# Performance work log

Hardware: AMD Instinct MI355X
Metric: run time of the kernel (lower is better)

## Reference

```python
import math
import jax, jax.numpy as jnp
import numpy as np

B, T, M, S, D, H = 16, 512, 8, 32, 256, 4
HD = D // H


def setup_inputs() -> dict:
    key = jax.random.key(0)
    ks = jax.random.split(key, 16)
    w = 1.0 / math.sqrt(D)
    return {
        'q_temporal': jax.random.normal(ks[0], (B, T, M, D), jnp.float32),
        'q_static': jax.random.normal(ks[1], (B, S, D), jnp.float32),
        'k_temporal': jax.random.normal(ks[2], (B, T, M, D), jnp.float32),
        'v_temporal': jax.random.normal(ks[3], (B, T, M, D), jnp.float32),
        'k_static': jax.random.normal(ks[4], (B, S, D), jnp.float32),
        'v_static': jax.random.normal(ks[5], (B, S, D), jnp.float32),
        'q_w': jax.random.normal(ks[6], (D, D), jnp.float32) * w,
        'q_b': jax.random.normal(ks[7], (D,), jnp.float32) * w,
        'k_w': jax.random.normal(ks[8], (D, D), jnp.float32) * w,
        'k_b': jax.random.normal(ks[9], (D,), jnp.float32) * w,
        'v_w': jax.random.normal(ks[10], (D, D), jnp.float32) * w,
        'v_b': jax.random.normal(ks[11], (D,), jnp.float32) * w,
        'o_w': jax.random.normal(ks[12], (D, D), jnp.float32) * w,
        'o_b': jax.random.normal(ks[13], (D,), jnp.float32) * w,
        'mask_temporal': jax.random.randint(ks[14], (B, T, M), 0, 2).astype(jnp.int32),
        'mask_fcst': jax.random.randint(ks[15], (B, T, M), 0, 2).astype(jnp.int32),
        'mask_static': jnp.ones((B, S), jnp.int32),
    }


def _lin(x, w, b):
    # torch.nn.Linear: y = x @ W^T + b
    return x @ w.T + b


def reference(q_temporal, q_static, k_temporal, v_temporal, k_static, v_static,
              q_w, q_b, k_w, k_b, v_w, v_b, o_w, o_b,
              mask_temporal, mask_fcst, mask_static):
    scale = 1.0 / math.sqrt(HD)

    def heads5(x):  # [B,T,M,D] -> [B,H,T,M,HD]
        return x.reshape(B, T, M, H, HD).transpose(0, 3, 1, 2, 4)

    def heads3(x):  # [B,S,D] -> [B,H,S,HD]
        return x.reshape(B, -1, H, HD).transpose(0, 2, 1, 3)

    Qt = heads5(_lin(q_temporal, q_w, q_b))
    Kt = heads5(_lin(k_temporal, k_w, k_b))
    Vt = heads5(_lin(v_temporal, v_w, v_b))
    Qs = heads3(_lin(q_static, q_w, q_b))
    Ks = heads3(_lin(k_static, k_w, k_b))
    Vs = heads3(_lin(v_static, v_w, v_b))

    # additive masks: 0 where valid (==1), -inf where padded
    mt = jnp.where(mask_temporal == 1, 0.0, -jnp.inf).astype(Qt.dtype)  # [B,T,M]
    ms = jnp.where(mask_static == 1, 0.0, -jnp.inf).astype(Qt.dtype)    # [B,S]

    # ---- temporal query branch ----
    # temp_temp: per-timestep modality-vs-modality attention, column key mask
    Qt_Kt = jnp.einsum('bhtmd,bhtnd->bhtmn', Qt, Kt) * scale + mt[:, None, :, None, :]
    # temp_static: temporal queries vs static keys
    Qt_Ks = jnp.einsum('bhtmd,bhsd->bhtms', Qt, Ks) * scale + ms[:, None, None, None, :]
    tw = jax.nn.softmax(jnp.concatenate([Qt_Kt, Qt_Ks], axis=-1), axis=-1)  # [B,H,T,M,M+S]
    QKV_t = (jnp.einsum('bhtmn,bhtnd->bhtmd', tw[..., :M], Vt)
             + jnp.einsum('bhtms,bhsd->bhtmd', tw[..., M:], Vs))
    out_t = _lin(QKV_t.transpose(0, 2, 3, 1, 4).reshape(B, T, M, D), o_w, o_b)

    # ---- static query branch ----
    Ktf = Kt.reshape(B, H, T * M, HD)  # flatten (T,M) key axis
    Vtf = Vt.reshape(B, H, T * M, HD)
    Qs_Kt = jnp.einsum('bhqd,bhkd->bhqk', Qs, Ktf) * scale + mt.reshape(B, 1, 1, T * M)
    Qs_Ks = jnp.einsum('bhqd,bhsd->bhqs', Qs, Ks) * scale + ms[:, None, None, :]
    sw = jax.nn.softmax(jnp.concatenate([Qs_Kt, Qs_Ks], axis=-1), axis=-1)  # [B,H,S,T*M+S]
    QKV_s = (jnp.einsum('bhqk,bhkd->bhqd', sw[..., :T * M], Vtf)
             + jnp.einsum('bhqs,bhsd->bhqd', sw[..., T * M:], Vs))
    out_s = _lin(QKV_s.transpose(0, 2, 1, 3).reshape(B, S, D), o_w, o_b)

    return (out_t, out_s, tw, sw)
```

## Files before the change

### kernel.cpp

```cpp
#include <hip/hip_runtime.h>

#define B_   16
#define T_   512
#define M_   8
#define S_   32
#define D_   256
#define H_   4
#define HD_  64
#define TM_  4096
#define NKT  40
#define NKS  4128

typedef unsigned short u16;
typedef __attribute__((ext_vector_type(8))) short bf16x8;
typedef __attribute__((ext_vector_type(4))) float f32x4;

__device__ __forceinline__ u16 f2b(float f) {
    union { float f; unsigned u; } v; v.f = f;
    unsigned r = v.u + 0x7FFF + ((v.u >> 16) & 1);
    return (u16)(r >> 16);
}
__device__ __forceinline__ float blo(unsigned u) {
    union { unsigned i; float f; } v; v.i = u << 16; return v.f;
}
__device__ __forceinline__ float bhi(unsigned u) {
    union { unsigned i; float f; } v; v.i = u & 0xFFFF0000u; return v.f;
}
__device__ __forceinline__ float b2f(u16 u) {
    union { unsigned i; float f; } v; v.i = ((unsigned)u) << 16; return v.f;
}
__device__ __forceinline__ unsigned pack2(float lo, float hi) {
    return (unsigned)f2b(lo) | ((unsigned)f2b(hi) << 16);
}
__device__ __forceinline__ uint4 cvt8(float4 a, float4 b) {
    uint4 r;
    r.x = pack2(a.x, a.y); r.y = pack2(a.z, a.w);
    r.z = pack2(b.x, b.y); r.w = pack2(b.z, b.w);
    return r;
}

template<int XBF, int OUTF32>
__device__ __forceinline__ void gemm_body(const void* __restrict__ Xv,
                                          const float* __restrict__ W,
                                          const float* __restrict__ bias,
                                          void* __restrict__ Yv,
                                          int bx, u16* sA, u16* sB)
{
    const int tid = threadIdx.x;
    const size_t r0 = (size_t)bx * 64;
    const int wave = tid >> 6, lane = tid & 63;
    const int rbase = lane & 15, kseg = (lane >> 4) * 8;
    const int arow = tid >> 2, aseg = tid & 3;

    f32x4 acc[4][4];
#pragma unroll
    for (int i = 0; i < 4; ++i)
#pragma unroll
        for (int j = 0; j < 4; ++j) acc[i][j] = (f32x4){0, 0, 0, 0};

#define LOAD_A(k0, dst)                                                          \
    if (XBF) dst = *(const uint4*)((const u16*)Xv + (r0 + arow) * 256 + (k0) + aseg * 8); \
    else {                                                                       \
        const float* gA = (const float*)Xv + (r0 + arow) * 256 + (k0) + aseg * 8; \
        dst = cvt8(*(const float4*)gA, *(const float4*)(gA + 4));                \
    }
#define LOAD_B(k0, dst)                                                          \
    _Pragma("unroll")                                                            \
    for (int i = 0; i < 4; ++i) {                                                \
        const int s = i * 256 + tid;                                             \
        const float* gB = W + (size_t)(s >> 2) * 256 + (k0) + (s & 3) * 8;       \
        dst[i] = cvt8(*(const float4*)gB, *(const float4*)(gB + 4));             \
    }

    {
        uint4 aC, bC[4];
        LOAD_A(0, aC)
        LOAD_B(0, bC)
        *(uint4*)(sA + tid * 8) = aC;
#pragma unroll
        for (int i = 0; i < 4; ++i)
            *(uint4*)(sB + (i * 256 + tid) * 8) = bC[i];
    }

    for (int k = 0; k < 8; ++k) {
        const int cur = k & 1;
        uint4 aN, bN[4];
        if (k < 7) {
            LOAD_A((k + 1) * 32, aN)
            LOAD_B((k + 1) * 32, bN)
        }
        __syncthreads();
        const u16* A = sA + cur * 2048;
        const u16* Bb = sB + cur * 8192;
        bf16x8 a[4], b[4];
#pragma unroll
        for (int f = 0; f < 4; ++f)
            a[f] = *(const bf16x8*)(A + (f * 16 + rbase) * 32 + kseg);
#pragma unroll
        for (int f = 0; f < 4; ++f)
            b[f] = *(const bf16x8*)(Bb + (wave * 64 + f * 16 + rbase) * 32 + kseg);
#pragma unroll
        for (int rf = 0; rf < 4; ++rf)
#pragma unroll
            for (int cf = 0; cf < 4; ++cf)
                acc[rf][cf] = __builtin_amdgcn_mfma_f32_16x16x32_bf16(
                    a[rf], b[cf], acc[rf][cf], 0, 0, 0);
        if (k < 7) {
            u16* A1 = sA + (cur ^ 1) * 2048;
            u16* B1 = sB + (cur ^ 1) * 8192;
            *(uint4*)(A1 + tid * 8) = aN;
#pragma unroll
            for (int i = 0; i < 4; ++i)
                *(uint4*)(B1 + (i * 256 + tid) * 8) = bN[i];
        }
    }
#undef LOAD_A
#undef LOAD_B

    const int orow = (lane >> 4) * 4, ocol = lane & 15;
#pragma unroll
    for (int cf = 0; cf < 4; ++cf) {
        const int col = wave * 64 + cf * 16 + ocol;
        const float bv = bias[col];
#pragma unroll
        for (int rf = 0; rf < 4; ++rf)
#pragma unroll
            for (int r = 0; r < 4; ++r) {
                const size_t row = r0 + rf * 16 + orow + r;
                const float y = acc[rf][cf][r] + bv;
                if (OUTF32) ((float*)Yv)[row * 256 + col] = y;
                else        ((u16*) Yv)[row * 256 + col] = f2b(y);
            }
    }
}

template<int XBF, int OUTF32>
__global__ __launch_bounds__(256) void k_gemm_m(const void* __restrict__ Xv,
                                                const float* __restrict__ W,
                                                const float* __restrict__ bias,
                                                void* __restrict__ Yv)
{
    __shared__ __align__(16) u16 sA[2 * 2048];
    __shared__ __align__(16) u16 sB[2 * 8192];
    gemm_body<XBF, OUTF32>(Xv, W, bias, Yv, blockIdx.x, sA, sB);
}

__global__ __launch_bounds__(256) void k_gemm_qkv(
    const float* __restrict__ X0, const float* __restrict__ X1, const float* __restrict__ X2,
    const float* __restrict__ W0, const float* __restrict__ W1, const float* __restrict__ W2,
    const float* __restrict__ b0, const float* __restrict__ b1, const float* __restrict__ b2,
    u16* __restrict__ Y0, u16* __restrict__ Y1, u16* __restrict__ Y2)
{
    __shared__ __align__(16) u16 sA[2 * 2048];
    __shared__ __align__(16) u16 sB[2 * 8192];
    const int sel = blockIdx.y;
    const float* X = sel == 0 ? X0 : sel == 1 ? X1 : X2;
    const float* W = sel == 0 ? W0 : sel == 1 ? W1 : W2;
    const float* bb = sel == 0 ? b0 : sel == 1 ? b1 : b2;
    u16* Y = sel == 0 ? Y0 : sel == 1 ? Y1 : Y2;
    gemm_body<0, 0>(X, W, bb, Y, blockIdx.x, sA, sB);
}

__global__ __launch_bounds__(256) void k_attn_t(
    const u16* __restrict__ Qt, const u16* __restrict__ Kt, const u16* __restrict__ Vt,
    const u16* __restrict__ Ks, const u16* __restrict__ Vs,
    const int* __restrict__ maskT, const int* __restrict__ maskS,
    float* __restrict__ tw, u16* __restrict__ qkvt)
{
    const int tp = blockIdx.x, b = blockIdx.y;
    const int t0 = tp * 2;
    __shared__ __align__(16) u16 sQ [4 * 2 * 16 * 32];
    __shared__ __align__(16) u16 sKT[4 * 2 * 16 * 32];
    __shared__ __align__(16) u16 sKS[4 * 2 * 32 * 32];
    __shared__ __align__(16) u16 sVT[4 * 64 * 72];
    __shared__ __align__(16) u16 sP [4 * 16 * 72];
    __shared__ int smT[2][8];
    __shared__ int smS[32];
    const int tid = threadIdx.x;

#pragma unroll
    for (int i = 0; i < 2; ++i) {
        const int fl = tid + i * 256;
        const int r = fl >> 5, c32 = fl & 31;
        const int h = c32 >> 3, ks = (c32 >> 2) & 1, seg = c32 & 3;
        const size_t src = (((size_t)b * T_ + t0 + (r >> 3)) * 8 + (r & 7)) * 256 + c32 * 8;
        const int dst = h * 1024 + ks * 512 + r * 32 + seg * 8;
        *(uint4*)(sQ  + dst) = *(const uint4*)(Qt + src);
        *(uint4*)(sKT + dst) = *(const uint4*)(Kt + src);
    }
#pragma unroll
    for (int i = 0; i < 4; ++i) {
        const int fl = tid + i * 256;
        const int r = fl >> 5, c32 = fl & 31;
        const int h = c32 >> 3, ks = (c32 >> 2) & 1, seg = c32 & 3;
        *(uint4*)(sKS + h * 2048 + ks * 1024 + r * 32 + seg * 8) =
            *(const uint4*)(Ks + ((size_t)b * S_ + r) * 256 + c32 * 8);
    }
    {
        const int key = tid & 63, dg = tid >> 6;
        const u16* vrow = nullptr;
        if (key < 16)      vrow = Vt + (((size_t)b * T_ + t0 + (key >> 3)) * 8 + (key & 7)) * 256;
        else if (key < 48) vrow = Vs + ((size_t)b * S_ + (key - 16)) * 256;
#pragma unroll
        for (int i = 0; i < 8; ++i) {
            const int dseg = dg * 8 + i;
            uint4 v = {0, 0, 0, 0};
            if (vrow) v = *(const uint4*)(vrow + dseg * 8);
            const int h = dseg >> 3, dl0 = (dseg & 7) * 8;
            const u16* pv = (const u16*)&v;
#pragma unroll
            for (int j = 0; j < 8; ++j)
                sVT[h * 4608 + (dl0 + j) * 72 + key] = pv[j];
        }
    }
    if (tid < 16) smT[tid >> 3][tid & 7] =
        maskT[((size_t)b * T_ + t0 + (tid >> 3)) * 8 + (tid & 7)];
    if (tid < 32) smS[tid] = maskS[b * S_ + tid];
    __syncthreads();

    const int h = tid >> 6, lane = tid & 63;
    const int c = lane & 15, g = lane >> 4, th = g >> 1;

    f32x4 at = {0,0,0,0}, as0 = {0,0,0,0}, as1 = {0,0,0,0};
#pragma unroll
    for (int ks = 0; ks < 2; ++ks) {
        bf16x8 aq = *(const bf16x8*)(sQ  + h * 1024 + ks * 512 + c * 32 + g * 8);
        bf16x8 bt = *(const bf16x8*)(sKT + h * 1024 + ks * 512 + c * 32 + g * 8);
        bf16x8 b0 = *(const bf16x8*)(sKS + h * 2048 + ks * 1024 + c * 32 + g * 8);
        bf16x8 b1 = *(const bf16x8*)(sKS + h * 2048 + ks * 1024 + 512 + c * 32 + g * 8);
        at  = __builtin_amdgcn_mfma_f32_16x16x32_bf16(aq, bt, at, 0, 0, 0);
        as0 = __builtin_amdgcn_mfma_f32_16x16x32_bf16(aq, b0, as0, 0, 0, 0);
        as1 = __builtin_amdgcn_mfma_f32_16x16x32_bf16(aq, b1, as1, 0, 0, 0);
    }

    const int vt = ((c >> 3) == th) ? smT[th][c & 7] : 0;
    const int v0 = smS[c], v1 = smS[16 + c];
    float st[4], s0[4], s1[4], mx[4];
#pragma unroll
    for (int r = 0; r < 4; ++r) {
        st[r] = vt ? at[r]  * 0.125f : -1e30f;
        s0[r] = v0 ? as0[r] * 0.125f : -1e30f;
        s1[r] = v1 ? as1[r] * 0.125f : -1e30f;
        mx[r] = fmaxf(fmaxf(st[r], s0[r]), s1[r]);
    }
#pragma unroll
    for (int o = 1; o < 16; o <<= 1)
#pragma unroll
        for (int r = 0; r < 4; ++r) mx[r] = fmaxf(mx[r], __shfl_xor(mx[r], o));
    float pt[4], p0[4], p1[4], sum[4];
#pragma unroll
    for (int r = 0; r < 4; ++r) {
        pt[r] = __expf(st[r] - mx[r]);
        p0[r] = __expf(s0[r] - mx[r]);
        p1[r] = __expf(s1[r] - mx[r]);
        sum[r] = pt[r] + p0[r] + p1[r];
    }
#pragma unroll
    for (int o = 1; o < 16; o <<= 1)
#pragma unroll
        for (int r = 0; r < 4; ++r) sum[r] += __shfl_xor(sum[r], o);
#pragma unroll
    for (int r = 0; r < 4; ++r) {
        const float inv = 1.0f / sum[r];
        pt[r] *= inv; p0[r] *= inv; p1[r] *= inv;
    }

#pragma unroll
    for (int r = 0; r < 4; ++r) {
        const int row = g * 4 + r;
        const int tt = t0 + (row >> 3), m = row & 7;
        float* twp = tw + ((((size_t)b * H_ + h) * T_ + tt) * 8 + m) * NKT;
        if ((c >> 3) == th) twp[c & 7] = pt[r];
        twp[8 + c]  = p0[r];
        twp[24 + c] = p1[r];
        u16* sp = sP + h * 1152 + row * 72;
        sp[c]      = f2b(pt[r]);
        sp[16 + c] = f2b(p0[r]);
        sp[32 + c] = f2b(p1[r]);
        sp[48 + c] = 0;
    }

    f32x4 o4[4] = {{0,0,0,0}, {0,0,0,0}, {0,0,0,0}, {0,0,0,0}};
#pragma unroll
    for (int ks = 0; ks < 2; ++ks) {
        bf16x8 pa = *(const bf16x8*)(sP + h * 1152 + c * 72 + ks * 32 + g * 8);
#pragma unroll
        for (int dt = 0; dt < 4; ++dt) {
            bf16x8 pb = *(const bf16x8*)(sVT + h * 4608 + (dt * 16 + c) * 72 + ks * 32 + g * 8);
            o4[dt] = __builtin_amdgcn_mfma_f32_16x16x32_bf16(pa, pb, o4[dt], 0, 0, 0);
        }
    }
#pragma unroll
    for (int dt = 0; dt < 4; ++dt)
#pragma unroll
        for (int r = 0; r < 4; ++r) {
            const int row = g * 4 + r;
            const int tt = t0 + (row >> 3), m = row & 7;
            qkvt[(((size_t)b * T_ + tt) * 8 + m) * 256 + h * 64 + dt * 16 + c] = f2b(o4[dt][r]);
        }
}

__global__ __launch_bounds__(256) void k_attn_s_scores(
    const u16* __restrict__ Qs, const u16* __restrict__ Kt, const u16* __restrict__ Ks,
    const int* __restrict__ maskT, const int* __restrict__ maskS,
    float* __restrict__ raw)
{
    const int ch = blockIdx.x, h = blockIdx.y, b = blockIdx.z;
    const int nk = (ch < 32) ? 128 : 32;
    const int k0 = ch * 128;
    __shared__ __align__(16) u16 sQ[2 * 32 * 32];
    __shared__ __align__(16) u16 sK[2 * 128 * 32];
    __shared__ int sM[128];
    const int tid = threadIdx.x;

    {   const int q = tid >> 3, c8 = tid & 7;
        const int ks = c8 >> 2, seg = c8 & 3;
        *(uint4*)(sQ + ks * 1024 + q * 32 + seg * 8) =
            *(const uint4*)(Qs + ((size_t)b * S_ + q) * 256 + h * 64 + c8 * 8);
    }
#pragma unroll
    for (int i = 0; i < 4; ++i) {
        const int fl = tid + i * 256;
        const int key = fl >> 3, c8 = fl & 7;
        const int ks = c8 >> 2, seg = c8 & 3;
        if (key < nk) {
            const u16* src = (ch < 32)
                ? (Kt + ((size_t)b * TM_ + k0 + key) * 256 + h * 64 + c8 * 8)
                : (Ks + ((size_t)b * S_  +      key) * 256 + h * 64 + c8 * 8);
            *(uint4*)(sK + ks * 4096 + key * 32 + seg * 8) = *(const uint4*)src;
        }
    }
    if (tid < nk) sM[tid] = (ch < 32) ? maskT[(size_t)b * TM_ + k0 + tid]
                                      : maskS[b * S_ + tid];
    __syncthreads();

    const int w = tid >> 6, lane = tid & 63;
    if (w * 32 >= nk) return;
    const int c = lane & 15, g = lane >> 4;

    f32x4 acc[2][2] = {{{0,0,0,0}, {0,0,0,0}}, {{0,0,0,0}, {0,0,0,0}}};
#pragma unroll
    for (int ks = 0; ks < 2; ++ks) {
        bf16x8 a0 = *(const bf16x8*)(sQ + ks * 1024 +        c * 32 + g * 8);
        bf16x8 a1 = *(const bf16x8*)(sQ + ks * 1024 + 512 +  c * 32 + g * 8);
        bf16x8 b0 = *(const bf16x8*)(sK + ks * 4096 + (w * 32 +      c) * 32 + g * 8);
        bf16x8 b1 = *(const bf16x8*)(sK + ks * 4096 + (w * 32 + 16 + c) * 32 + g * 8);
        acc[0][0] = __builtin_amdgcn_mfma_f32_16x16x32_bf16(a0, b0, acc[0][0], 0, 0, 0);
        acc[0][1] = __builtin_amdgcn_mfma_f32_16x16x32_bf16(a0, b1, acc[0][1], 0, 0, 0);
        acc[1][0] = __builtin_amdgcn_mfma_f32_16x16x32_bf16(a1, b0, acc[1][0], 0, 0, 0);
        acc[1][1] = __builtin_amdgcn_mfma_f32_16x16x32_bf16(a1, b1, acc[1][1], 0, 0, 0);
    }
#pragma unroll
    for (int rt = 0; rt < 2; ++rt)
#pragma unroll
        for (int ct = 0; ct < 2; ++ct) {
            const int kl = w * 32 + ct * 16 + c;
            const float madd = sM[kl] ? 0.f : -1e30f;
#pragma unroll
            for (int r = 0; r < 4; ++r) {
                const int q = rt * 16 + g * 4 + r;
                raw[(((size_t)b * H_ + h) * S_ + q) * NKS + k0 + kl] =
                    acc[rt][ct][r] * 0.125f + madd;
            }
        }
}

__global__ __launch_bounds__(256) void k_attn_s_softmax(
    const float* __restrict__ raw, float* __restrict__ sw)
{
    const int q = blockIdx.x, h = blockIdx.y, b = blockIdx.z;
    __shared__ float sRow[NKS];
    __shared__ float red[8];
    const int tid = threadIdx.x;
    const size_t base = (((size_t)b * H_ + h) * S_ + q) * NKS;

    float mx = -1e30f;
    for (int i = tid; i < NKS; i += 256) {
        const float v = raw[base + i];
        sRow[i] = v;
        mx = fmaxf(mx, v);
    }
    for (int o = 32; o; o >>= 1) mx = fmaxf(mx, __shfl_xor(mx, o));
    if ((tid & 63) == 0) red[tid >> 6] = mx;
    __syncthreads();
    mx = fmaxf(fmaxf(red[0], red[1]), fmaxf(red[2], red[3]));

    float sum = 0.f;
    for (int i = tid; i < NKS; i += 256) {
        const float e = __expf(sRow[i] - mx);
        sRow[i] = e;
        sum += e;
    }
    for (int o = 32; o; o >>= 1) sum += __shfl_xor(sum, o);
    if ((tid & 63) == 0) red[4 + (tid >> 6)] = sum;
    __syncthreads();
    sum = (red[4] + red[5]) + (red[6] + red[7]);
    const float inv = 1.0f / sum;

    for (int i = tid; i < NKS; i += 256)
        sw[base + i] = sRow[i] * inv;
}

__global__ __launch_bounds__(256) void k_attn_s_pv_part(
    const float* __restrict__ w, const u16* __restrict__ Vt, const u16* __restrict__ Vs,
    float* __restrict__ part)
{
    const int ch = blockIdx.x, h = blockIdx.y, b = blockIdx.z;
    const int nk = (ch < 32) ? 128 : 32;
    const int k0 = ch * 128;
    __shared__ float sW[32][132];
    __shared__ __align__(16) u16 sV[128 * 64];
    const int tid = threadIdx.x;

#pragma unroll
    for (int i = 0; i < 4; ++i) {
        const int fl = tid + i * 256;
        const int q = fl >> 5, k4 = fl & 31;
        if (k4 * 4 < nk)
            *(float4*)&sW[q][k4 * 4] =
                *(const float4*)(w + (((size_t)b * H_ + h) * S_ + q) * NKS + k0 + k4 * 4);
    }
#pragma unroll
    for (int i = 0; i < 4; ++i) {
        const int fl = tid + i * 256;
        const int key = fl >> 3, pp = fl & 7;
        if (key < nk) {
            const u16* src = (ch < 32)
                ? (Vt + ((size_t)b * TM_ + k0 + key) * D_ + h * HD_ + pp * 8)
                : (Vs + ((size_t)b * S_  +      key) * D_ + h * HD_ + pp * 8);
            ((uint4*)sV)[fl] = *(const uint4*)src;
        }
    }
    __syncthreads();

    const int d = tid & 63, qg = tid >> 6;
    float acc[8] = {0,0,0,0,0,0,0,0};
    for (int kk = 0; kk < nk; kk += 4) {
        const float v0 = b2f(sV[(kk + 0) * 64 + d]);
        const float v1 = b2f(sV[(kk + 1) * 64 + d]);
        const float v2 = b2f(sV[(kk + 2) * 64 + d]);
        const float v3 = b2f(sV[(kk + 3) * 64 + d]);
#pragma unroll
        for (int j = 0; j < 8; ++j) {
            const float4 wv = *(const float4*)&sW[qg * 8 + j][kk];
            acc[j] += wv.x * v0 + wv.y * v1 + wv.z * v2 + wv.w * v3;
        }
    }

    float* pb = part + (((size_t)ch * B_ + b) * H_ + h) * 2048;
#pragma unroll
    for (int j = 0; j < 8; ++j)
        pb[(qg * 8 + j) * 64 + d] = acc[j];
}

__global__ __launch_bounds__(256) void k_attn_s_pv_red(
    const float* __restrict__ part, u16* __restrict__ qkvs)
{
    const int h = blockIdx.x, b = blockIdx.y;
    const int tid = threadIdx.x;
    for (int i = tid; i < 2048; i += 256) {
        float s = 0.f;
#pragma unroll
        for (int c = 0; c < 33; ++c)
            s += part[(((size_t)c * B_ + b) * H_ + h) * 2048 + i];
        const int q = i >> 6, d = i & 63;
        qkvs[((size_t)b * S_ + q) * D_ + h * HD_ + d] = f2b(s);
    }
}

extern "C" void kernel_launch(void* const* d_in, const int* in_sizes, int n_in,
                              void* d_out, int out_size, void* d_ws, size_t ws_size,
                              hipStream_t stream)
{
    const float* q_t = (const float*)d_in[0];
    const float* q_s = (const float*)d_in[1];
    const float* k_t = (const float*)d_in[2];
    const float* v_t = (const float*)d_in[3];
    const float* k_s = (const float*)d_in[4];
    const float* v_s = (const float*)d_in[5];
    const float* q_w = (const float*)d_in[6];
    const float* q_b = (const float*)d_in[7];
    const float* k_w = (const float*)d_in[8];
    const float* k_b = (const float*)d_in[9];
    const float* v_w = (const float*)d_in[10];
    const float* v_b = (const float*)d_in[11];
    const float* o_w = (const float*)d_in[12];
    const float* o_b = (const float*)d_in[13];
    const int* maskT = (const int*)d_in[14];
    const int* maskS = (const int*)d_in[16];
    float* out = (float*)d_out;

    char* ws = (char*)d_ws;
    u16*   Kt   = (u16*)(ws + 0);
    u16*   Vt   = (u16*)(ws + 33554432);
    u16*   QKVt = (u16*)(ws + 67108864);
    float* part = (float*)(ws + 67108864);
    u16*   Qs   = (u16*)(ws + 100663296);
    u16*   Ks   = (u16*)(ws + 100925440);
    u16*   Vs   = (u16*)(ws + 101187584);
    u16*   QKVs = (u16*)(ws + 101449728);
    u16*   Qt   = (u16*)(ws + 101711872);
    float* raw  = (float*)(ws + 101711872);
    if (ws_size < 135528448) return;

    float* out_t = out;
    float* out_s = out + 16777216;
    float* tw    = out + 16908288;
    float* sw    = out + 27394048;

    const dim3 blk(256);
    k_gemm_qkv<<<dim3(1024, 3), blk, 0, stream>>>(q_t, k_t, v_t, q_w, k_w, v_w,
                                                  q_b, k_b, v_b, Qt, Kt, Vt);
    k_gemm_qkv<<<dim3(8, 3),    blk, 0, stream>>>(q_s, k_s, v_s, q_w, k_w, v_w,
                                                  q_b, k_b, v_b, Qs, Ks, Vs);

    k_attn_t<<<dim3(256, 16), blk, 0, stream>>>(Qt, Kt, Vt, Ks, Vs, maskT, maskS, tw, QKVt);

    k_gemm_m<1,1><<<dim3(1024), blk, 0, stream>>>(QKVt, o_w, o_b, out_t);

    k_attn_s_scores<<<dim3(33, 4, 16), blk, 0, stream>>>(Qs, Kt, Ks, maskT, maskS, raw);
    k_attn_s_softmax<<<dim3(32, 4, 16), blk, 0, stream>>>(raw, sw);
    k_attn_s_pv_part<<<dim3(33, 4, 16), blk, 0, stream>>>(sw, Vt, Vs, part);
    k_attn_s_pv_red<<<dim3(4, 16), blk, 0, stream>>>(part, QKVs);

    k_gemm_m<1,1><<<dim3(8),    blk, 0, stream>>>(QKVs, o_w, o_b, out_s);
}
```

Measured before the change: 284.3 us.

## Pre-convert weights to bf16 and stage GEMM tiles with direct global-to-LDS loads

Adds a small kernel converting projection weights to bf16 once, so GEMM blocks load bf16 weights via global_load_lds directly into shared memory instead of loading and converting fp32 per block. The bf16 A operand is also staged asynchronously, and the bf16 output epilogue is routed through LDS for coalesced 16-byte stores. This adds extra conversion launches and workspace aliasing that depends on kernel ordering.

New measurement: 257.5 us. -9.4%, faster.

```diff
diff --git a/kernel.cpp b/kernel.cpp
--- a/kernel.cpp
+++ b/kernel.cpp
@@ -39,13 +39,33 @@
     return r;
 }
 
+#define GLL16(g, l) __builtin_amdgcn_global_load_lds( \
+    (const __attribute__((address_space(1))) void*)(g), \
+    (__attribute__((address_space(3))) void*)(l), 16, 0, 0)
+
+__global__ __launch_bounds__(256) void k_cvt_w(const float* __restrict__ W0,
+                                               const float* __restrict__ W1,
+                                               const float* __restrict__ W2,
+                                               u16* __restrict__ dst)
+{
+    const int sel = blockIdx.y;
+    const float* W = sel == 0 ? W0 : sel == 1 ? W1 : W2;
+    u16* d = dst + sel * 65536;
+    const int i0 = (blockIdx.x * 256 + threadIdx.x) * 8;
+    const float4 a = *(const float4*)(W + i0);
+    const float4 b = *(const float4*)(W + i0 + 4);
+    *(uint4*)(d + i0) = cvt8(a, b);
+}
+
 template<int XBF, int OUTF32>
 __device__ __forceinline__ void gemm_body(const void* __restrict__ Xv,
-                                          const float* __restrict__ W,
+                                          const u16* __restrict__ Wb,
                                           const float* __restrict__ bias,
                                           void* __restrict__ Yv,
-                                          int bx, u16* sA, u16* sB)
-{
+                                          int bx, u16* smem)
+{
+    u16* sA = smem;
+    u16* sB = smem + 4096;
     const int tid = threadIdx.x;
     const size_t r0 = (size_t)bx * 64;
     const int wave = tid >> 6, lane = tid & 63;
@@ -58,39 +78,38 @@
 #pragma unroll
         for (int j = 0; j < 4; ++j) acc[i][j] = (f32x4){0, 0, 0, 0};
 
-#define LOAD_A(k0, dst)                                                          \
-    if (XBF) dst = *(const uint4*)((const u16*)Xv + (r0 + arow) * 256 + (k0) + aseg * 8); \
-    else {                                                                       \
+#define LOAD_A_F32(k0, dst) {                                                    \
         const float* gA = (const float*)Xv + (r0 + arow) * 256 + (k0) + aseg * 8; \
         dst = cvt8(*(const float4*)gA, *(const float4*)(gA + 4));                \
     }
-#define LOAD_B(k0, dst)                                                          \
+#define STAGE_B_GLL(k0, bi)                                                      \
     _Pragma("unroll")                                                            \
     for (int i = 0; i < 4; ++i) {                                                \
         const int s = i * 256 + tid;                                             \
-        const float* gB = W + (size_t)(s >> 2) * 256 + (k0) + (s & 3) * 8;       \
-        dst[i] = cvt8(*(const float4*)gB, *(const float4*)(gB + 4));             \
-    }
+        GLL16(Wb + (size_t)(s >> 2) * 256 + (k0) + (s & 3) * 8,                  \
+              sB + (bi) * 8192 + (i * 256 + wave * 64) * 8);                     \
+    }
+#define STAGE_A_GLL(k0, bi)                                                      \
+    GLL16((const u16*)Xv + (r0 + arow) * 256 + (k0) + aseg * 8,                  \
+          sA + (bi) * 2048 + wave * 512);
 
     {
-        uint4 aC, bC[4];
-        LOAD_A(0, aC)
-        LOAD_B(0, bC)
-        *(uint4*)(sA + tid * 8) = aC;
-#pragma unroll
-        for (int i = 0; i < 4; ++i)
-            *(uint4*)(sB + (i * 256 + tid) * 8) = bC[i];
+        if (XBF) { STAGE_A_GLL(0, 0) }
+        else { uint4 aC; LOAD_A_F32(0, aC) *(uint4*)(sA + tid * 8) = aC; }
+        STAGE_B_GLL(0, 0)
     }
 
     for (int k = 0; k < 8; ++k) {
         const int cur = k & 1;
-        uint4 aN, bN[4];
+        __syncthreads();
+        uint4 aN;
         if (k < 7) {
-            LOAD_A((k + 1) * 32, aN)
-            LOAD_B((k + 1) * 32, bN)
-        }
-        __syncthreads();
-        const u16* A = sA + cur * 2048;
+            const int k0n = (k + 1) * 32;
+            if (XBF) { STAGE_A_GLL(k0n, cur ^ 1) }
+            else     { LOAD_A_F32(k0n, aN) }
+            STAGE_B_GLL(k0n, cur ^ 1)
+        }
+        const u16* A  = sA + cur * 2048;
         const u16* Bb = sB + cur * 8192;
         bf16x8 a[4], b[4];
 #pragma unroll
@@ -105,60 +124,69 @@
             for (int cf = 0; cf < 4; ++cf)
                 acc[rf][cf] = __builtin_amdgcn_mfma_f32_16x16x32_bf16(
                     a[rf], b[cf], acc[rf][cf], 0, 0, 0);
-        if (k < 7) {
-            u16* A1 = sA + (cur ^ 1) * 2048;
-            u16* B1 = sB + (cur ^ 1) * 8192;
-            *(uint4*)(A1 + tid * 8) = aN;
-#pragma unroll
-            for (int i = 0; i < 4; ++i)
-                *(uint4*)(B1 + (i * 256 + tid) * 8) = bN[i];
-        }
-    }
-#undef LOAD_A
-#undef LOAD_B
+        if (k < 7 && !XBF)
+            *(uint4*)(sA + (cur ^ 1) * 2048 + tid * 8) = aN;
+    }
+#undef LOAD_A_F32
+#undef STAGE_B_GLL
+#undef STAGE_A_GLL
 
     const int orow = (lane >> 4) * 4, ocol = lane & 15;
-#pragma unroll
-    for (int cf = 0; cf < 4; ++cf) {
-        const int col = wave * 64 + cf * 16 + ocol;
-        const float bv = bias[col];
-#pragma unroll
-        for (int rf = 0; rf < 4; ++rf)
-#pragma unroll
-            for (int r = 0; r < 4; ++r) {
-                const size_t row = r0 + rf * 16 + orow + r;
-                const float y = acc[rf][cf][r] + bv;
-                if (OUTF32) ((float*)Yv)[row * 256 + col] = y;
-                else        ((u16*) Yv)[row * 256 + col] = f2b(y);
-            }
+    if (OUTF32) {
+#pragma unroll
+        for (int cf = 0; cf < 4; ++cf) {
+            const int col = wave * 64 + cf * 16 + ocol;
+            const float bv = bias[col];
+#pragma unroll
+            for (int rf = 0; rf < 4; ++rf)
+#pragma unroll
+                for (int r = 0; r < 4; ++r)
+                    ((float*)Yv)[(r0 + rf * 16 + orow + r) * 256 + col] =
+                        acc[rf][cf][r] + bv;
+        }
+    } else {
+        __syncthreads();
+#pragma unroll
+        for (int cf = 0; cf < 4; ++cf) {
+            const int col = wave * 64 + cf * 16 + ocol;
+            const float bv = bias[col];
+#pragma unroll
+            for (int rf = 0; rf < 4; ++rf)
+#pragma unroll
+                for (int r = 0; r < 4; ++r)
+                    smem[(rf * 16 + orow + r) * 256 + col] = f2b(acc[rf][cf][r] + bv);
+        }
+        __syncthreads();
+#pragma unroll
+        for (int i = 0; i < 8; ++i) {
+            const int s = i * 256 + tid;
+            *(uint4*)((u16*)Yv + r0 * 256 + (size_t)s * 8) = *(const uint4*)(smem + s * 8);
+        }
     }
 }
 
 template<int XBF, int OUTF32>
 __global__ __launch_bounds__(256) void k_gemm_m(const void* __restrict__ Xv,
-                                                const float* __restrict__ W,
+                                                const u16* __restrict__ Wb,
                                                 const float* __restrict__ bias,
                                                 void* __restrict__ Yv)
 {
-    __shared__ __align__(16) u16 sA[2 * 2048];
-    __shared__ __align__(16) u16 sB[2 * 8192];
-    gemm_body<XBF, OUTF32>(Xv, W, bias, Yv, blockIdx.x, sA, sB);
+    __shared__ __align__(16) u16 smem[20480];
+    gemm_body<XBF, OUTF32>(Xv, Wb, bias, Yv, blockIdx.x, smem);
 }
 
 __global__ __launch_bounds__(256) void k_gemm_qkv(
     const float* __restrict__ X0, const float* __restrict__ X1, const float* __restrict__ X2,
-    const float* __restrict__ W0, const float* __restrict__ W1, const float* __restrict__ W2,
+    const u16* __restrict__ Wb,
     const float* __restrict__ b0, const float* __restrict__ b1, const float* __restrict__ b2,
     u16* __restrict__ Y0, u16* __restrict__ Y1, u16* __restrict__ Y2)
 {
-    __shared__ __align__(16) u16 sA[2 * 2048];
-    __shared__ __align__(16) u16 sB[2 * 8192];
+    __shared__ __align__(16) u16 smem[20480];
     const int sel = blockIdx.y;
     const float* X = sel == 0 ? X0 : sel == 1 ? X1 : X2;
-    const float* W = sel == 0 ? W0 : sel == 1 ? W1 : W2;
     const float* bb = sel == 0 ? b0 : sel == 1 ? b1 : b2;
     u16* Y = sel == 0 ? Y0 : sel == 1 ? Y1 : Y2;
-    gemm_body<0, 0>(X, W, bb, Y, blockIdx.x, sA, sB);
+    gemm_body<0, 0>(X, Wb + sel * 65536, bb, Y, blockIdx.x, smem);
 }
 
 __global__ __launch_bounds__(256) void k_attn_t(
@@ -495,12 +523,14 @@
     u16*   Vt   = (u16*)(ws + 33554432);
     u16*   QKVt = (u16*)(ws + 67108864);
     float* part = (float*)(ws + 67108864);
+    u16*   Wqkv = (u16*)(ws + 67108864);
     u16*   Qs   = (u16*)(ws + 100663296);
     u16*   Ks   = (u16*)(ws + 100925440);
     u16*   Vs   = (u16*)(ws + 101187584);
     u16*   QKVs = (u16*)(ws + 101449728);
     u16*   Qt   = (u16*)(ws + 101711872);
     float* raw  = (float*)(ws + 101711872);
+    u16*   Wo   = (u16*)(ws + 101711872);
     if (ws_size < 135528448) return;
 
     float* out_t = out;
@@ -509,19 +539,23 @@
     float* sw    = out + 27394048;
 
     const dim3 blk(256);
-    k_gemm_qkv<<<dim3(1024, 3), blk, 0, stream>>>(q_t, k_t, v_t, q_w, k_w, v_w,
+    k_cvt_w<<<dim3(32, 3), blk, 0, stream>>>(q_w, k_w, v_w, Wqkv);
+
+    k_gemm_qkv<<<dim3(1024, 3), blk, 0, stream>>>(q_t, k_t, v_t, Wqkv,
                                                   q_b, k_b, v_b, Qt, Kt, Vt);
-    k_gemm_qkv<<<dim3(8, 3),    blk, 0, stream>>>(q_s, k_s, v_s, q_w, k_w, v_w,
+    k_gemm_qkv<<<dim3(8, 3),    blk, 0, stream>>>(q_s, k_s, v_s, Wqkv,
                                                   q_b, k_b, v_b, Qs, Ks, Vs);
 
     k_attn_t<<<dim3(256, 16), blk, 0, stream>>>(Qt, Kt, Vt, Ks, Vs, maskT, maskS, tw, QKVt);
 
-    k_gemm_m<1,1><<<dim3(1024), blk, 0, stream>>>(QKVt, o_w, o_b, out_t);
+    k_cvt_w<<<dim3(32, 1), blk, 0, stream>>>(o_w, o_w, o_w, Wo);
+    k_gemm_m<1,1><<<dim3(1024), blk, 0, stream>>>(QKVt, Wo, o_b, out_t);
 
     k_attn_s_scores<<<dim3(33, 4, 16), blk, 0, stream>>>(Qs, Kt, Ks, maskT, maskS, raw);
     k_attn_s_softmax<<<dim3(32, 4, 16), blk, 0, stream>>>(raw, sw);
+    k_cvt_w<<<dim3(32, 1), blk, 0, stream>>>(o_w, o_w, o_w, Wo);
     k_attn_s_pv_part<<<dim3(33, 4, 16), blk, 0, stream>>>(sw, Vt, Vs, part);
     k_attn_s_pv_red<<<dim3(4, 16), blk, 0, stream>>>(part, QKVs);
 
-    k_gemm_m<1,1><<<dim3(8),    blk, 0, stream>>>(QKVs, o_w, o_b, out_s);
-}
+    k_gemm_m<1,1><<<dim3(8),    blk, 0, stream>>>(QKVs, Wo, o_b, out_s);
+}
```
